# Performance work log

Measured on AMD Instinct MI355X. Metric: run time of the kernel, lower is better.

The kernel has to match this reference:

```python
import jax, jax.numpy as jnp
import numpy as np

N_VERTS = 35709  # BFM mesh vertices; bases have 3*N_VERTS rows
LANDMARK_INDEX = np.array([27440, 27208, 27608, 27816, 35472, 34766, 34312, 34022, 33838, 33654, 33375, 32939, 32244, 16264, 16467, 16888, 16644, 31716, 31056, 30662, 30454, 30288, 29549, 29382, 29177, 28787, 28111, 8161, 8177, 8187, 8192, 9883, 9163, 8204, 7243, 6515, 14066, 12383, 11353, 10455, 11492, 12653, 5828, 4920, 3886, 2215, 3640, 4801, 10795, 10395, 8935, 8215, 7495, 6025, 5522, 6915, 7636, 8236, 8836, 9555, 10537, 9064, 8223, 7384, 5909, 7629, 8229, 8829], dtype=np.int32)
LANDMARK_WEIGHT = np.ones(68, dtype=np.float32)
LANDMARK_WEIGHT[17:27] = 50.0
LANDMARK_WEIGHT[36:68] = 50.0


def setup_inputs() -> dict:
    key = jax.random.key(0)
    ks = jax.random.split(key, 6)
    B = 64
    return {
        "alpha": jax.random.normal(ks[0], (B, 80, 1), dtype=jnp.float32),
        "delta": jax.random.normal(ks[1], (B, 64, 1), dtype=jnp.float32),
        "reference_alpha": jax.random.normal(ks[2], (B, 80, 1), dtype=jnp.float32),
        "delta_pred": jax.random.normal(ks[3], (B, 64, 1), dtype=jnp.float32),
        "id_base": jax.random.normal(ks[4], (3 * N_VERTS, 80), dtype=jnp.float32),
        "exp_base": jax.random.normal(ks[5], (3 * N_VERTS, 64), dtype=jnp.float32),
    }


def _geo(id_base, exp_base, a, d):
    # batched matvec: [V3, K] x [B, K] -> [B, V3]; reshape to [B, 35709, 3]
    g = jnp.einsum('vk,bk->bv', id_base, a[..., 0]) + jnp.einsum('vk,bk->bv', exp_base, d[..., 0])
    return g.reshape(-1, N_VERTS, 3)


def reference(alpha, delta, reference_alpha, delta_pred, id_base, exp_base):
    lm_idx = jnp.asarray(LANDMARK_INDEX)
    w = jnp.asarray(LANDMARK_WEIGHT)[None, :, None]  # [1, 68, 1]
    geo_gt = _geo(id_base, exp_base, alpha, delta)[:, lm_idx]          # [B, 68, 3]
    geo_pred = _geo(id_base, exp_base, reference_alpha, delta_pred)[:, lm_idx]
    l2 = (geo_gt - geo_pred) ** 2
    return jnp.sum(w * l2) / 68.0
```

## Files before the change

### kernel.cpp

```cpp
#include <hip/hip_runtime.h>
#include <hip/hip_bf16.h>


#define NUM_LM 68
#define K_ID 80
#define K_EXP 64
#define NROWS 204
#define NWAVES 7
#define MT 2
#define BLOCK (NWAVES * 64)
#define CD_STRIDE 168

typedef short bf16x8 __attribute__((ext_vector_type(8)));
typedef float f32x4  __attribute__((ext_vector_type(4)));

__device__ __constant__ int LM_IDX[NUM_LM] = {
    27440, 27208, 27608, 27816, 35472, 34766, 34312, 34022, 33838, 33654,
    33375, 32939, 32244, 16264, 16467, 16888, 16644, 31716, 31056, 30662,
    30454, 30288, 29549, 29382, 29177, 28787, 28111,  8161,  8177,  8187,
     8192,  9883,  9163,  8204,  7243,  6515, 14066, 12383, 11353, 10455,
    11492, 12653,  5828,  4920,  3886,  2215,  3640,  4801, 10795, 10395,
     8935,  8215,  7495,  6025,  5522,  6915,  7636,  8236,  8836,  9555,
    10537,  9064,  8223,  7384,  5909,  7629,  8229,  8829
};

__device__ __forceinline__ unsigned pk2(float x, float y) {
    __hip_bfloat162 h = __float22bfloat162_rn(float2{x, y});
    union { __hip_bfloat162 h; unsigned u; } c; c.h = h; return c.u;
}

__global__ __launch_bounds__(BLOCK) void fused_geo_loss(
        const float* __restrict__ alpha,
        const float* __restrict__ delta,
        const float* __restrict__ ref_alpha,
        const float* __restrict__ delta_pred,
        const float* __restrict__ id_base,
        const float* __restrict__ exp_base,
        float* __restrict__ out) {
    __shared__ __align__(16) unsigned short cdT[64 * CD_STRIDE];
    __shared__ float red[NWAVES];

    const int tid = threadIdx.x;
    const int w   = tid >> 6;
    const int l   = tid & 63;
    const int mh  = l & 15;
    const int g   = l >> 4;

    float4 af[MT][5][2];
    #pragma unroll
    for (int u = 0; u < MT; ++u) {
        const int  m     = 32 * w + 16 * u + mh;
        const bool valid = m < NROWS;
        const int  lmi   = valid ? (m / 3) : 0;
        const int  cc    = m - 3 * (m / 3);
        const long long vrow = 3LL * LM_IDX[lmi] + cc;
        const float* __restrict__ idp = id_base  + vrow * K_ID;
        const float* __restrict__ exq = exp_base + vrow * K_EXP;
        #pragma unroll
        for (int s = 0; s < 5; ++s) {
            const int k0 = 32 * s + g * 8;
            if (valid && k0 < K_ID) {
                af[u][s][0] = *(const float4*)(idp + k0);
                af[u][s][1] = *(const float4*)(idp + k0 + 4);
            } else if (valid && k0 < K_ID + K_EXP) {
                af[u][s][0] = *(const float4*)(exq + (k0 - K_ID));
                af[u][s][1] = *(const float4*)(exq + (k0 - K_ID) + 4);
            } else {
                af[u][s][0] = float4{0.f, 0.f, 0.f, 0.f};
                af[u][s][1] = float4{0.f, 0.f, 0.f, 0.f};
            }
        }
    }

    for (int i = tid; i < (64 * K_ID) / 8; i += BLOCK) {
        const int b = i / 10, k = 8 * (i - 10 * b);
        const float* ap = alpha     + b * K_ID + k;
        const float* rp = ref_alpha + b * K_ID + k;
        float4 a0 = *(const float4*)ap,       a1 = *(const float4*)(ap + 4);
        float4 r0 = *(const float4*)rp,       r1 = *(const float4*)(rp + 4);
        uint4 q;
        q.x = pk2(a0.x - r0.x, a0.y - r0.y);
        q.y = pk2(a0.z - r0.z, a0.w - r0.w);
        q.z = pk2(a1.x - r1.x, a1.y - r1.y);
        q.w = pk2(a1.z - r1.z, a1.w - r1.w);
        *(uint4*)&cdT[b * CD_STRIDE + k] = q;
    }
    for (int i = tid; i < (64 * K_EXP) / 8; i += BLOCK) {
        const int b = i >> 3, k = 8 * (i & 7);
        const float* dp = delta      + b * K_EXP + k;
        const float* qp = delta_pred + b * K_EXP + k;
        float4 d0 = *(const float4*)dp,       d1 = *(const float4*)(dp + 4);
        float4 e0 = *(const float4*)qp,       e1 = *(const float4*)(qp + 4);
        uint4 q;
        q.x = pk2(d0.x - e0.x, d0.y - e0.y);
        q.y = pk2(d0.z - e0.z, d0.w - e0.w);
        q.z = pk2(d1.x - e1.x, d1.y - e1.y);
        q.w = pk2(d1.z - e1.z, d1.w - e1.w);
        *(uint4*)&cdT[b * CD_STRIDE + K_ID + k] = q;
    }
    for (int i = tid; i < 64 * 2; i += BLOCK) {
        const int b = i >> 1, k = 144 + 8 * (i & 1);
        *(uint4*)&cdT[b * CD_STRIDE + k] = uint4{0u, 0u, 0u, 0u};
    }

    bf16x8 a[MT][5];
    #pragma unroll
    for (int u = 0; u < MT; ++u)
        #pragma unroll
        for (int s = 0; s < 5; ++s) {
            const float* fp = (const float*)&af[u][s][0];
            union { bf16x8 v; unsigned q[4]; } cv;
            #pragma unroll
            for (int j = 0; j < 4; ++j)
                cv.q[j] = pk2(fp[2 * j], fp[2 * j + 1]);
            a[u][s] = cv.v;
        }

    __syncthreads();

    f32x4 acc[MT][4];
    const f32x4 z4 = {0.f, 0.f, 0.f, 0.f};
    #pragma unroll
    for (int u = 0; u < MT; ++u)
        #pragma unroll
        for (int t = 0; t < 4; ++t) acc[u][t] = z4;

    #pragma unroll
    for (int s = 0; s < 5; ++s) {
        bf16x8 bfrag[4];
        #pragma unroll
        for (int t = 0; t < 4; ++t)
            bfrag[t] = *(const bf16x8*)&cdT[(16 * t + mh) * CD_STRIDE + 32 * s + g * 8];
        #pragma unroll
        for (int u = 0; u < MT; ++u)
            #pragma unroll
            for (int t = 0; t < 4; ++t)
                acc[u][t] = __builtin_amdgcn_mfma_f32_16x16x32_bf16(
                    a[u][s], bfrag[t], acc[u][t], 0, 0, 0);
    }

    float v = 0.f;
    #pragma unroll
    for (int u = 0; u < MT; ++u) {
        #pragma unroll
        for (int q = 0; q < 4; ++q) {
            const int row = 32 * w + 16 * u + 4 * g + q;
            float wq = 0.f;
            if (row < NROWS) {
                const int li = row / 3;
                wq = ((li >= 17 && li < 27) || li >= 36) ? 50.f : 1.f;
            }
            float sq = 0.f;
            #pragma unroll
            for (int t = 0; t < 4; ++t) sq += acc[u][t][q] * acc[u][t][q];
            v += wq * sq;
        }
    }
    #pragma unroll
    for (int off = 32; off; off >>= 1) v += __shfl_down(v, off, 64);
    if (l == 0) red[w] = v;
    __syncthreads();
    if (tid == 0) {
        float tot = 0.f;
        #pragma unroll
        for (int i = 0; i < NWAVES; ++i) tot += red[i];
        out[0] = tot * (1.0f / 68.0f);
    }
}

extern "C" void kernel_launch(void* const* d_in, const int* in_sizes, int n_in,
                              void* d_out, int out_size, void* d_ws, size_t ws_size,
                              hipStream_t stream) {
    const float* alpha      = (const float*)d_in[0];
    const float* delta      = (const float*)d_in[1];
    const float* ref_alpha  = (const float*)d_in[2];
    const float* delta_pred = (const float*)d_in[3];
    const float* id_base    = (const float*)d_in[4];
    const float* exp_base   = (const float*)d_in[5];
    float* out = (float*)d_out;

    fused_geo_loss<<<dim3(1), dim3(BLOCK), 0, stream>>>(
        alpha, delta, ref_alpha, delta_pred, id_base, exp_base, out);
}
```

Baseline: 11.59 us.

## Split fused landmark loss across four blocks with last-block reduction

The single-block kernel is split into four blocks, each taking half of the 204 landmark rows and half of the 64-sample batch, with four waves per block. Each block writes its partial sum to workspace, and the last block to arrive (tracked by an atomic counter) sums the partials and resets the counter. This spreads the scattered base-row loads and the MFMA work over more compute units to cut per-block latency. In exchange it adds atomics, memory fences and a global counter that must be reset correctly between launches.

```diff
diff --git a/kernel.cpp b/kernel.cpp
--- a/kernel.cpp
+++ b/kernel.cpp
@@ -6,7 +6,9 @@
 #define K_ID 80
 #define K_EXP 64
 #define NROWS 204
-#define NWAVES 7
+#define RHALF 102
+#define BHALF 32
+#define NWAVES 4
 #define MT 2
 #define BLOCK (NWAVES * 64)
 #define CD_STRIDE 168
@@ -24,6 +26,8 @@
     10537,  9064,  8223,  7384,  5909,  7629,  8229,  8829
 };
 
+__device__ unsigned gcnt = 0;
+
 __device__ __forceinline__ unsigned pk2(float x, float y) {
     __hip_bfloat162 h = __float22bfloat162_rn(float2{x, y});
     union { __hip_bfloat162 h; unsigned u; } c; c.h = h; return c.u;
@@ -36,8 +40,9 @@
         const float* __restrict__ delta_pred,
         const float* __restrict__ id_base,
         const float* __restrict__ exp_base,
+        float* __restrict__ ws,
         float* __restrict__ out) {
-    __shared__ __align__(16) unsigned short cdT[64 * CD_STRIDE];
+    __shared__ __align__(16) unsigned short cdT[BHALF * CD_STRIDE];
     __shared__ float red[NWAVES];
 
     const int tid = threadIdx.x;
@@ -45,14 +50,17 @@
     const int l   = tid & 63;
     const int mh  = l & 15;
     const int g   = l >> 4;
+    const int rb  = blockIdx.x >> 1;
+    const int bb  = blockIdx.x & 1;
 
     float4 af[MT][5][2];
     #pragma unroll
     for (int u = 0; u < MT; ++u) {
-        const int  m     = 32 * w + 16 * u + mh;
-        const bool valid = m < NROWS;
-        const int  lmi   = valid ? (m / 3) : 0;
-        const int  cc    = m - 3 * (m / 3);
+        const int  lr    = 32 * w + 16 * u + mh;
+        const bool valid = lr < RHALF;
+        const int  mg    = RHALF * rb + lr;
+        const int  lmi   = valid ? (mg / 3) : 0;
+        const int  cc    = mg - 3 * (mg / 3);
         const long long vrow = 3LL * LM_IDX[lmi] + cc;
         const float* __restrict__ idp = id_base  + vrow * K_ID;
         const float* __restrict__ exq = exp_base + vrow * K_EXP;
@@ -72,35 +80,37 @@
         }
     }
 
-    for (int i = tid; i < (64 * K_ID) / 8; i += BLOCK) {
-        const int b = i / 10, k = 8 * (i - 10 * b);
+    for (int i = tid; i < (BHALF * K_ID) / 8; i += BLOCK) {
+        const int lb = i / 10, k = 8 * (i - 10 * lb);
+        const int b  = BHALF * bb + lb;
         const float* ap = alpha     + b * K_ID + k;
         const float* rp = ref_alpha + b * K_ID + k;
-        float4 a0 = *(const float4*)ap,       a1 = *(const float4*)(ap + 4);
-        float4 r0 = *(const float4*)rp,       r1 = *(const float4*)(rp + 4);
+        float4 a0 = *(const float4*)ap, a1 = *(const float4*)(ap + 4);
+        float4 r0 = *(const float4*)rp, r1 = *(const float4*)(rp + 4);
         uint4 q;
         q.x = pk2(a0.x - r0.x, a0.y - r0.y);
         q.y = pk2(a0.z - r0.z, a0.w - r0.w);
         q.z = pk2(a1.x - r1.x, a1.y - r1.y);
         q.w = pk2(a1.z - r1.z, a1.w - r1.w);
-        *(uint4*)&cdT[b * CD_STRIDE + k] = q;
-    }
-    for (int i = tid; i < (64 * K_EXP) / 8; i += BLOCK) {
-        const int b = i >> 3, k = 8 * (i & 7);
+        *(uint4*)&cdT[lb * CD_STRIDE + k] = q;
+    }
+    for (int i = tid; i < (BHALF * K_EXP) / 8; i += BLOCK) {
+        const int lb = i >> 3, k = 8 * (i & 7);
+        const int b  = BHALF * bb + lb;
         const float* dp = delta      + b * K_EXP + k;
         const float* qp = delta_pred + b * K_EXP + k;
-        float4 d0 = *(const float4*)dp,       d1 = *(const float4*)(dp + 4);
-        float4 e0 = *(const float4*)qp,       e1 = *(const float4*)(qp + 4);
+        float4 d0 = *(const float4*)dp, d1 = *(const float4*)(dp + 4);
+        float4 e0 = *(const float4*)qp, e1 = *(const float4*)(qp + 4);
         uint4 q;
         q.x = pk2(d0.x - e0.x, d0.y - e0.y);
         q.y = pk2(d0.z - e0.z, d0.w - e0.w);
         q.z = pk2(d1.x - e1.x, d1.y - e1.y);
         q.w = pk2(d1.z - e1.z, d1.w - e1.w);
-        *(uint4*)&cdT[b * CD_STRIDE + K_ID + k] = q;
-    }
-    for (int i = tid; i < 64 * 2; i += BLOCK) {
-        const int b = i >> 1, k = 144 + 8 * (i & 1);
-        *(uint4*)&cdT[b * CD_STRIDE + k] = uint4{0u, 0u, 0u, 0u};
+        *(uint4*)&cdT[lb * CD_STRIDE + K_ID + k] = q;
+    }
+    for (int i = tid; i < BHALF * 2; i += BLOCK) {
+        const int lb = i >> 1, k = 144 + 8 * (i & 1);
+        *(uint4*)&cdT[lb * CD_STRIDE + k] = uint4{0u, 0u, 0u, 0u};
     }
 
     bf16x8 a[MT][5];
@@ -118,23 +128,21 @@
 
     __syncthreads();
 
-    f32x4 acc[MT][4];
+    f32x4 acc[MT][2];
     const f32x4 z4 = {0.f, 0.f, 0.f, 0.f};
     #pragma unroll
-    for (int u = 0; u < MT; ++u)
-        #pragma unroll
-        for (int t = 0; t < 4; ++t) acc[u][t] = z4;
+    for (int u = 0; u < MT; ++u) { acc[u][0] = z4; acc[u][1] = z4; }
 
     #pragma unroll
     for (int s = 0; s < 5; ++s) {
-        bf16x8 bfrag[4];
-        #pragma unroll
-        for (int t = 0; t < 4; ++t)
+        bf16x8 bfrag[2];
+        #pragma unroll
+        for (int t = 0; t < 2; ++t)
             bfrag[t] = *(const bf16x8*)&cdT[(16 * t + mh) * CD_STRIDE + 32 * s + g * 8];
         #pragma unroll
         for (int u = 0; u < MT; ++u)
             #pragma unroll
-            for (int t = 0; t < 4; ++t)
+            for (int t = 0; t < 2; ++t)
                 acc[u][t] = __builtin_amdgcn_mfma_f32_16x16x32_bf16(
                     a[u][s], bfrag[t], acc[u][t], 0, 0, 0);
     }
@@ -144,15 +152,15 @@
     for (int u = 0; u < MT; ++u) {
         #pragma unroll
         for (int q = 0; q < 4; ++q) {
-            const int row = 32 * w + 16 * u + 4 * g + q;
+            const int lr = 32 * w + 16 * u + 4 * g + q;
             float wq = 0.f;
-            if (row < NROWS) {
-                const int li = row / 3;
+            if (lr < RHALF) {
+                const int li = (RHALF * rb + lr) / 3;
                 wq = ((li >= 17 && li < 27) || li >= 36) ? 50.f : 1.f;
             }
             float sq = 0.f;
             #pragma unroll
-            for (int t = 0; t < 4; ++t) sq += acc[u][t][q] * acc[u][t][q];
+            for (int t = 0; t < 2; ++t) sq += acc[u][t][q] * acc[u][t][q];
             v += wq * sq;
         }
     }
@@ -160,11 +168,22 @@
     for (int off = 32; off; off >>= 1) v += __shfl_down(v, off, 64);
     if (l == 0) red[w] = v;
     __syncthreads();
+
     if (tid == 0) {
-        float tot = 0.f;
-        #pragma unroll
-        for (int i = 0; i < NWAVES; ++i) tot += red[i];
-        out[0] = tot * (1.0f / 68.0f);
+        const float p = (red[0] + red[1]) + (red[2] + red[3]);
+        atomicExch(&ws[blockIdx.x], p);
+        __threadfence();
+        const unsigned old = atomicAdd(&gcnt, 1u);
+        if (old == 3u) {
+            __threadfence();
+            float tot = 0.f;
+            #pragma unroll
+            for (int i = 0; i < 4; ++i)
+                tot += atomicAdd(&ws[i], 0.0f);
+            out[0] = tot * (1.0f / 68.0f);
+            __threadfence();
+            gcnt = 0;
+        }
     }
 }
 
@@ -178,7 +197,8 @@
     const float* id_base    = (const float*)d_in[4];
     const float* exp_base   = (const float*)d_in[5];
     float* out = (float*)d_out;
-
-    fused_geo_loss<<<dim3(1), dim3(BLOCK), 0, stream>>>(
-        alpha, delta, ref_alpha, delta_pred, id_base, exp_base, out);
+    float* ws  = (float*)d_ws;
+
+    fused_geo_loss<<<dim3(4), dim3(BLOCK), 0, stream>>>(
+        alpha, delta, ref_alpha, delta_pred, id_base, exp_base, ws, out);
 }
```

Result: no change. 11.68 us (+0.7%).
